# Performance work log

Hardware: AMD Instinct MI355X
Metric: run time of the kernel (lower is better)

The kernel has to match this reference:

```python
import jax, jax.numpy as jnp
import numpy as np

EPS_ATTN = 1e-6
EPS_LN = 1e-5


def _layer_norm(x, g, b):
    m = jnp.mean(x, axis=-1, keepdims=True)
    v = jnp.mean((x - m) ** 2, axis=-1, keepdims=True)
    return (x - m) * jax.lax.rsqrt(v + EPS_LN) * g + b


def _linear_attention(q, k, v):
    # q,k,v: [N, L/S, H, D]; elu feature map (+1 keeps values positive)
    q = jax.nn.elu(q) + 1.0
    k = jax.nn.elu(k) + 1.0
    s_len = v.shape[1]
    v = v / s_len
    kv = jnp.einsum('nshd,nshv->nhdv', k, v)            # [N,H,D,D]
    z = 1.0 / (jnp.einsum('nlhd,nhd->nlh', q, k.sum(axis=1)) + EPS_ATTN)
    out = jnp.einsum('nlhd,nhdv->nlhv', q, kv) * z[..., None] * s_len
    return out


def setup_inputs() -> dict:
    key = jax.random.key(0)
    ks = jax.random.split(key, 8)
    N, L, S, H, D = 4, 4096, 4096, 8, 64
    sc = 0.05
    return {
        'x': jax.random.normal(ks[0], (N, L, H, D), jnp.float32),
        'source': jax.random.normal(ks[1], (N, S, H, D), jnp.float32),
        'wq': jax.random.normal(ks[2], (D, D), jnp.float32) * sc,
        'wk': jax.random.normal(ks[3], (D, D), jnp.float32) * sc,
        'wv': jax.random.normal(ks[4], (D, D), jnp.float32) * sc,
        'wmerge': jax.random.normal(ks[5], (D, D), jnp.float32) * sc,
        'w1': jax.random.normal(ks[6], (2 * D, 2 * D), jnp.float32) * sc,
        'w2': jax.random.normal(ks[7], (D, 2 * D), jnp.float32) * sc,
        'g1': jnp.ones((D,), jnp.float32),
        'b1': jnp.zeros((D,), jnp.float32),
        'g2': jnp.ones((D,), jnp.float32),
        'b2': jnp.zeros((D,), jnp.float32),
    }


def reference(x, source, wq, wk, wv, wmerge, w1, w2, g1, b1, g2, b2):
    # projections (torch Linear: y = x @ W.T), applied on last dim D=d_model
    q = jnp.einsum('nlhd,ed->nlhe', x, wq)
    k = jnp.einsum('nshd,ed->nshe', source, wk)
    v = jnp.einsum('nshd,ed->nshe', source, wv)
    message = _linear_attention(q, k, v)                # [N,L,H,D]
    message = jnp.einsum('nlhd,ed->nlhe', message, wmerge)
    message = _layer_norm(message, g1, b1)
    h = jnp.concatenate([x, message], axis=-1)          # [N,L,H,2D]
    h = jax.nn.relu(jnp.einsum('nlhd,ed->nlhe', h, w1))
    h = jnp.einsum('nlhd,ed->nlhe', h, w2)              # [N,L,H,D]
    h = _layer_norm(h, g2, b2)
    return x + h
```

## Files before the change

### kernel.cpp

```cpp
#include <hip/hip_runtime.h>
#include <cstdint>

#define NB 4
#define LL 4096
#define SS 4096
#define HH 8
#define DD 64
#define NHC (NB*HH)
#define KVCH 16

typedef unsigned short ushort_t;
typedef __bf16 bf16x8 __attribute__((ext_vector_type(8)));
typedef float f32x4 __attribute__((ext_vector_type(4)));
typedef unsigned short u16x8 __attribute__((ext_vector_type(8)));
typedef unsigned short u16x4 __attribute__((ext_vector_type(4)));

__device__ __forceinline__ float bf2f(unsigned short u) {
    union { unsigned int i; float f; } v; v.i = ((unsigned int)u) << 16; return v.f;
}
__device__ __forceinline__ unsigned short f2bf(float f) {
    union { __bf16 b; unsigned short u; } v; v.b = (__bf16)f; return v.u;
}
__device__ __forceinline__ bool input_is_bf16(const void* g1) {
    return ((const unsigned short*)g1)[0] == 0x3F80u;
}

template<bool BF16>
__device__ __forceinline__ float ldgf(const void* p, size_t i) {
    if constexpr (BF16) return bf2f(((const unsigned short*)p)[i]);
    else                return ((const float*)p)[i];
}
template<bool BF16>
__device__ __forceinline__ u16x8 ld8(const void* p, size_t i) {
    if constexpr (BF16) {
        return *reinterpret_cast<const u16x8*>((const unsigned short*)p + i);
    } else {
        const f32x4* f4 = reinterpret_cast<const f32x4*>((const float*)p + i);
        f32x4 a = f4[0], b = f4[1];
        u16x8 o;
        #pragma unroll
        for (int j = 0; j < 4; ++j) { o[j] = f2bf(a[j]); o[4 + j] = f2bf(b[j]); }
        return o;
    }
}
__device__ __forceinline__ bf16x8 ldsA(const ushort_t* p) {
    return *reinterpret_cast<const bf16x8*>(p);
}
#define MFMA16(a,b,c) __builtin_amdgcn_mfma_f32_16x16x32_bf16(a,b,c,0,0,0)

__device__ __forceinline__ int sw64(int r, int c)  { return (r << 6) + (c ^ ((r & 7) << 3)); }
__device__ __forceinline__ int sw128(int r, int c) { return (r << 7) + (c ^ ((r & 7) << 3)); }

template<bool BF16, int LC>
__device__ __forceinline__ void stage_w(const void* g, size_t goff, ushort_t* dst,
                                        int rows, int dstride, int tid) {
    int total8 = (rows << LC) >> 3;
    for (int i8 = tid; i8 < total8; i8 += 256) {
        int i = i8 << 3;
        int r = i >> LC, c = i & ((1 << LC) - 1);
        *reinterpret_cast<u16x8*>(dst + r * dstride + c) = ld8<BF16>(g, goff + i);
    }
}
template<bool BF16, int LC, int NT>
__device__ __forceinline__ void stage_sw(const void* g, ushort_t* dst, int rows, int tid) {
    int total8 = (rows << LC) >> 3;
    for (int i8 = tid; i8 < total8; i8 += NT) {
        int i = i8 << 3;
        int r = i >> LC, c = i & ((1 << LC) - 1);
        int off;
        if constexpr (LC == 6) off = sw64(r, c); else off = sw128(r, c);
        *reinterpret_cast<u16x8*>(dst + off) = ld8<BF16>(g, i);
    }
}

__device__ __forceinline__ void red16(float v[4]) {
    #pragma unroll
    for (int m = 1; m < 16; m <<= 1) {
        #pragma unroll
        for (int r = 0; r < 4; ++r) v[r] += __shfl_xor(v[r], m);
    }
}

template<bool BF16, bool PART>
__device__ void kv_body(const void* __restrict__ src, const void* __restrict__ wk,
                        const void* __restrict__ wv, float* __restrict__ kvg,
                        float* __restrict__ ksumg,
                        ushort_t* S, ushort_t* KT, ushort_t* VT, float* KS)
{
    const int tid = threadIdx.x;
    const int lane = tid & 63, w = tid >> 6;
    const int lg = lane >> 4, l15 = lane & 15;
    const int bid = blockIdx.x;
    const int nh = bid >> 4, ch = bid & 15;
    const int n = nh >> 3, h = nh & 7;
    const int s0 = ch * 256;
    const f32x4 z4 = {0.f, 0.f, 0.f, 0.f};

    stage_w<BF16, 6>(wk, 0, KT, 64, 136, tid);
    stage_w<BF16, 6>(wv, 0, VT, 64, 136, tid);
    for (int i8 = tid; i8 < 1024; i8 += 256) {
        int r = i8 >> 3, c8 = (i8 & 7) << 3;
        size_t gb = ((size_t)((size_t)n * SS + (s0 + r)) * HH + h) * DD + c8;
        *reinterpret_cast<u16x8*>(S + r * 72 + c8) = ld8<BF16>(src, gb);
    }
    __syncthreads();

    bf16x8 wkf[2][4], wvf[2][4];
    #pragma unroll
    for (int ks = 0; ks < 2; ++ks)
        #pragma unroll
        for (int nt = 0; nt < 4; ++nt) {
            wkf[ks][nt] = ldsA(KT + (nt * 16 + l15) * 136 + ks * 32 + lg * 8);
            wvf[ks][nt] = ldsA(VT + (nt * 16 + l15) * 136 + ks * 32 + lg * 8);
        }
    __syncthreads();

    f32x4 kvacc[4];
    #pragma unroll
    for (int nt = 0; nt < 4; ++nt) kvacc[nt] = z4;
    float ksp[4] = {0.f, 0.f, 0.f, 0.f};

    for (int st = 0; st < 2; ++st) {
        #pragma unroll
        for (int mtt = 0; mtt < 2; ++mtt) {
            const int rowA = w * 32 + mtt * 16;
            bf16x8 af[2];
            #pragma unroll
            for (int ks = 0; ks < 2; ++ks)
                af[ks] = ldsA(S + (rowA + l15) * 72 + ks * 32 + lg * 8);
            f32x4 ka[4], va[4];
            #pragma unroll
            for (int nt = 0; nt < 4; ++nt) { ka[nt] = z4; va[nt] = z4; }
            __builtin_amdgcn_s_setprio(1);
            #pragma unroll
            for (int ks = 0; ks < 2; ++ks)
                #pragma unroll
                for (int nt = 0; nt < 4; ++nt) {
                    ka[nt] = MFMA16(af[ks], wkf[ks][nt], ka[nt]);
                    va[nt] = MFMA16(af[ks], wvf[ks][nt], va[nt]);
                }
            __builtin_amdgcn_s_setprio(0);
            #pragma unroll
            for (int nt = 0; nt < 4; ++nt) {
                u16x4 kp, vp;
                #pragma unroll
                for (int r = 0; r < 4; ++r) {
                    float kvl = ka[nt][r];
                    kvl = kvl > 0.f ? kvl + 1.f : __expf(kvl);
                    ksp[nt] += kvl;
                    kp[r] = f2bf(kvl);
                    vp[r] = f2bf(va[nt][r]);
                }
                const int dcol = nt * 16 + l15;
                *reinterpret_cast<u16x4*>(KT + dcol * 136 + rowA + lg * 4) = kp;
                *reinterpret_cast<u16x4*>(VT + dcol * 136 + rowA + lg * 4) = vp;
            }
        }
        __syncthreads();

        if (st == 0) {
            for (int i8 = tid; i8 < 1024; i8 += 256) {
                int r = i8 >> 3, c8 = (i8 & 7) << 3;
                size_t gb = ((size_t)((size_t)n * SS + (s0 + 128 + r)) * HH + h) * DD + c8;
                *reinterpret_cast<u16x8*>(S + r * 72 + c8) = ld8<BF16>(src, gb);
            }
        }
        __builtin_amdgcn_s_setprio(1);
        #pragma unroll
        for (int ks = 0; ks < 4; ++ks) {
            bf16x8 akv = ldsA(KT + (w * 16 + l15) * 136 + ks * 32 + lg * 8);
            #pragma unroll
            for (int nt = 0; nt < 4; ++nt) {
                bf16x8 bkv = ldsA(VT + (nt * 16 + l15) * 136 + ks * 32 + lg * 8);
                kvacc[nt] = MFMA16(akv, bkv, kvacc[nt]);
            }
        }
        __builtin_amdgcn_s_setprio(0);
        __syncthreads();
    }

    if constexpr (PART) {
        float* kvo = kvg + (size_t)bid * 4096;
        #pragma unroll
        for (int nt = 0; nt < 4; ++nt)
            #pragma unroll
            for (int r = 0; r < 4; ++r)
                kvo[(w * 16 + lg * 4 + r) * DD + nt * 16 + l15] = kvacc[nt][r];
    } else {
        float* kvo = kvg + (size_t)nh * 4096;
        #pragma unroll
        for (int nt = 0; nt < 4; ++nt)
            #pragma unroll
            for (int r = 0; r < 4; ++r)
                atomicAdd(&kvo[(w * 16 + lg * 4 + r) * DD + nt * 16 + l15], kvacc[nt][r]);
    }
    #pragma unroll
    for (int m = 16; m < 64; m <<= 1)
        #pragma unroll
        for (int nt = 0; nt < 4; ++nt) ksp[nt] += __shfl_xor(ksp[nt], m);
    if (lane < 16) {
        #pragma unroll
        for (int nt = 0; nt < 4; ++nt) KS[w * 64 + nt * 16 + lane] = ksp[nt];
    }
    __syncthreads();
    if (tid < 64) {
        float s = KS[tid] + KS[64 + tid] + KS[128 + tid] + KS[192 + tid];
        if constexpr (PART) ksumg[(size_t)bid * 64 + tid] = s;
        else                atomicAdd(&ksumg[nh * 64 + tid], s);
    }
}

template<bool PART>
__global__ __launch_bounds__(256, 2) void kv_kernel(
    const void* __restrict__ src, const void* __restrict__ wk, const void* __restrict__ wv,
    const void* __restrict__ g1, float* __restrict__ kvg, float* __restrict__ ksumg)
{
    __shared__ ushort_t S[128 * 72];
    __shared__ ushort_t KT[64 * 136];
    __shared__ ushort_t VT[64 * 136];
    __shared__ float    KS[4 * 64];
    if (input_is_bf16(g1)) kv_body<true , PART>(src, wk, wv, kvg, ksumg, S, KT, VT, KS);
    else                   kv_body<false, PART>(src, wk, wv, kvg, ksumg, S, KT, VT, KS);
}

template<bool BF16, int NCH>
__device__ void reduce_body(const float* __restrict__ kvp, const float* __restrict__ ksp,
                            const void* __restrict__ wm,
                            ushort_t* __restrict__ kvmT, float* __restrict__ ksumf,
                            ushort_t* KVS, ushort_t* WMS)
{
    const int tid = threadIdx.x;
    const int lane = tid & 63, w = tid >> 6;
    const int lg = lane >> 4, l15 = lane & 15;
    const int nh = blockIdx.x;
    const f32x4 z4 = {0.f, 0.f, 0.f, 0.f};

    stage_w<BF16, 6>(wm, 0, WMS, 64, 72, tid);
    for (int i4 = tid; i4 < 1024; i4 += 256) {
        const float* base = kvp + (size_t)nh * NCH * 4096 + i4 * 4;
        f32x4 s = z4;
        #pragma unroll
        for (int c = 0; c < NCH; ++c)
            s += *reinterpret_cast<const f32x4*>(base + c * 4096);
        int d = i4 >> 4, e4 = (i4 & 15) * 4;
        u16x4 pk;
        #pragma unroll
        for (int j = 0; j < 4; ++j) pk[j] = f2bf(s[j]);
        *reinterpret_cast<u16x4*>(KVS + d * 72 + e4) = pk;
    }
    if (tid < 64) {
        float s = 0.f;
        #pragma unroll
        for (int c = 0; c < NCH; ++c) s += ksp[((size_t)nh * NCH + c) * 64 + tid];
        ksumf[nh * 64 + tid] = s;
    }
    __syncthreads();

    bf16x8 akv[2];
    #pragma unroll
    for (int ks = 0; ks < 2; ++ks)
        akv[ks] = ldsA(KVS + (w * 16 + l15) * 72 + ks * 32 + lg * 8);
    f32x4 km[4];
    #pragma unroll
    for (int nt = 0; nt < 4; ++nt) km[nt] = z4;
    #pragma unroll
    for (int ks = 0; ks < 2; ++ks)
        #pragma unroll
        for (int nt = 0; nt < 4; ++nt) {
            bf16x8 bwm = ldsA(WMS + (nt * 16 + l15) * 72 + ks * 32 + lg * 8);
            km[nt] = MFMA16(akv[ks], bwm, km[nt]);
        }
    #pragma unroll
    for (int nt = 0; nt < 4; ++nt) {
        u16x4 pk;
        #pragma unroll
        for (int r = 0; r < 4; ++r) pk[r] = f2bf(km[nt][r]);
        *reinterpret_cast<u16x4*>(kvmT + (size_t)nh * 4096 + (nt * 16 + l15) * 64
                                  + w * 16 + lg * 4) = pk;
    }
}

template<int NCH>
__global__ __launch_bounds__(256, 4) void reduce_kernel(
    const float* __restrict__ kvp, const float* __restrict__ ksp,
    const void* __restrict__ wm, const void* __restrict__ g1,
    ushort_t* __restrict__ kvmT, float* __restrict__ ksumf)
{
    __shared__ ushort_t KVS[64 * 72];
    __shared__ ushort_t WMS[64 * 72];
    if (input_is_bf16(g1)) reduce_body<true , NCH>(kvp, ksp, wm, kvmT, ksumf, KVS, WMS);
    else                   reduce_body<false, NCH>(kvp, ksp, wm, kvmT, ksumf, KVS, WMS);
}

template<bool BF16>
__device__ void main_body(const void* __restrict__ x,
                          const void* __restrict__ wq,
                          const void* __restrict__ w1, const void* __restrict__ w2,
                          const void* __restrict__ g1, const void* __restrict__ b1,
                          const void* __restrict__ g2, const void* __restrict__ b2,
                          const ushort_t* __restrict__ kvmT,
                          const float* __restrict__ ksumf,
                          void* __restrict__ outp,
                          ushort_t* W1S, ushort_t* W2S, ushort_t* WQS,
                          ushort_t* KVMS, ushort_t* B0, ushort_t* B1, ushort_t* B2)
{
    const int tid = threadIdx.x;
    const int lane = tid & 63, w = tid >> 6;
    const int lg = lane >> 4, l15 = lane & 15;
    const int bid = blockIdx.x;
    const int nh = bid >> 3, ch = bid & 7;
    const int n = nh >> 3, h = nh & 7;
    const int rowA = w * 16;
    const f32x4 z4 = {0.f, 0.f, 0.f, 0.f};

    auto ldx = [&](int p, u16x8 xv[2]) {
        #pragma unroll
        for (int pp = 0; pp < 2; ++pp) {
            int r16 = pp * 8 + (lane >> 3), c8 = (lane & 7) << 3;
            size_t gb = ((size_t)((size_t)n * LL + (ch * 512 + p * 256 + rowA + r16)) * HH + h) * DD + c8;
            xv[pp] = ld8<BF16>(x, gb);
        }
    };

    u16x8 xv[2];
    ldx(0, xv);

    stage_sw<BF16, 6, 1024>(wq, WQS, 64, tid);
    stage_sw<BF16, 7, 1024>(w2, W2S, 64, tid);
    stage_sw<BF16, 7, 1024>(w1, W1S, 128, tid);
    stage_sw<true, 6, 1024>((const void*)(kvmT + (size_t)nh * 4096), KVMS, 64, tid);
    float g1r[4], b1r[4], g2r[4], b2r[4], ksr[4];
    #pragma unroll
    for (int nt = 0; nt < 4; ++nt) {
        int c = nt * 16 + l15;
        g1r[nt] = ldgf<BF16>(g1, c); b1r[nt] = ldgf<BF16>(b1, c);
        g2r[nt] = ldgf<BF16>(g2, c); b2r[nt] = ldgf<BF16>(b2, c);
        ksr[nt] = ksumf[nh * 64 + c];
    }
    __syncthreads();

    for (int p = 0; p < 2; ++p) {
        const int l0 = ch * 512 + p * 256;

        #pragma unroll
        for (int pp = 0; pp < 2; ++pp) {
            int r16 = pp * 8 + (lane >> 3), c8 = (lane & 7) << 3;
            *reinterpret_cast<u16x8*>(B0 + sw64(rowA + r16, c8)) = xv[pp];
        }
        u16x8 xn[2];
        if (p == 0) ldx(1, xn);

        bf16x8 af[2];
        #pragma unroll
        for (int ks = 0; ks < 2; ++ks)
            af[ks] = ldsA(B0 + sw64(rowA + l15, ks * 32 + lg * 8));
        f32x4 qa[4];
        #pragma unroll
        for (int nt = 0; nt < 4; ++nt) qa[nt] = z4;
        __builtin_amdgcn_s_setprio(1);
        #pragma unroll
        for (int ks = 0; ks < 2; ++ks)
            #pragma unroll
            for (int nt = 0; nt < 4; ++nt)
                qa[nt] = MFMA16(af[ks], ldsA(WQS + sw64(nt * 16 + l15, ks * 32 + lg * 8)), qa[nt]);
        __builtin_amdgcn_s_setprio(0);
        float zp[4] = {0.f, 0.f, 0.f, 0.f};
        #pragma unroll
        for (int nt = 0; nt < 4; ++nt)
            #pragma unroll
            for (int r = 0; r < 4; ++r) {
                float v = qa[nt][r];
                v = v > 0.f ? v + 1.f : __expf(v);
                zp[r] += v * ksr[nt];
                B1[sw64(rowA + lg * 4 + r, nt * 16 + l15)] = f2bf(v);
            }
        red16(zp);
        float zr[4];
        #pragma unroll
        for (int r = 0; r < 4; ++r) zr[r] = 1.f / (zp[r] + 1e-6f);

        #pragma unroll
        for (int ks = 0; ks < 2; ++ks)
            af[ks] = ldsA(B1 + sw64(rowA + l15, ks * 32 + lg * 8));
        f32x4 ma[4];
        #pragma unroll
        for (int nt = 0; nt < 4; ++nt) ma[nt] = z4;
        __builtin_amdgcn_s_setprio(1);
        #pragma unroll
        for (int ks = 0; ks < 2; ++ks)
            #pragma unroll
            for (int nt = 0; nt < 4; ++nt)
                ma[nt] = MFMA16(af[ks], ldsA(KVMS + sw64(nt * 16 + l15, ks * 32 + lg * 8)), ma[nt]);
        __builtin_amdgcn_s_setprio(0);
        #pragma unroll
        for (int nt = 0; nt < 4; ++nt)
            #pragma unroll
            for (int r = 0; r < 4; ++r) ma[nt][r] *= zr[r];

        float s1[4] = {0.f,0.f,0.f,0.f}, s2[4] = {0.f,0.f,0.f,0.f};
        #pragma unroll
        for (int nt = 0; nt < 4; ++nt)
            #pragma unroll
            for (int r = 0; r < 4; ++r) {
                float v = ma[nt][r]; s1[r] += v; s2[r] += v * v;
            }
        red16(s1); red16(s2);
        #pragma unroll
        for (int r = 0; r < 4; ++r) {
            float mu = s1[r] * 0.015625f;
            float var = s2[r] * 0.015625f - mu * mu;
            s1[r] = mu; s2[r] = rsqrtf(var + 1e-5f);
        }
        #pragma unroll
        for (int nt = 0; nt < 4; ++nt)
            #pragma unroll
            for (int r = 0; r < 4; ++r)
                B1[sw64(rowA + lg * 4 + r, nt * 16 + l15)] =
                    f2bf((ma[nt][r] - s1[r]) * s2[r] * g1r[nt] + b1r[nt]);

        f32x4 ha[4];
        #pragma unroll
        for (int nt = 0; nt < 4; ++nt) ha[nt] = z4;
        #pragma unroll
        for (int q = 0; q < 4; ++q) {
            f32x4 ta[2];
            ta[0] = z4; ta[1] = z4;
            __builtin_amdgcn_s_setprio(1);
            #pragma unroll
            for (int ks = 0; ks < 4; ++ks) {
                const ushort_t* bp = (ks < 2) ? B0 : B1;
                bf16x8 a1 = ldsA(bp + sw64(rowA + l15, (ks & 1) * 32 + lg * 8));
                #pragma unroll
                for (int nt = 0; nt < 2; ++nt)
                    ta[nt] = MFMA16(a1, ldsA(W1S + sw128(q * 32 + nt * 16 + l15, ks * 32 + lg * 8)), ta[nt]);
            }
            __builtin_amdgcn_s_setprio(0);
            #pragma unroll
            for (int nt = 0; nt < 2; ++nt)
                #pragma unroll
                for (int r = 0; r < 4; ++r)
                    B2[(rowA + lg * 4 + r) * 40 + nt * 16 + l15] =
                        f2bf(fmaxf(ta[nt][r], 0.f));
            bf16x8 a2 = ldsA(B2 + (rowA + l15) * 40 + lg * 8);
            __builtin_amdgcn_s_setprio(1);
            #pragma unroll
            for (int nt = 0; nt < 4; ++nt)
                ha[nt] = MFMA16(a2, ldsA(W2S + sw128(nt * 16 + l15, q * 32 + lg * 8)), ha[nt]);
            __builtin_amdgcn_s_setprio(0);
        }

        float t1[4] = {0.f,0.f,0.f,0.f}, t2[4] = {0.f,0.f,0.f,0.f};
        #pragma unroll
        for (int nt = 0; nt < 4; ++nt)
            #pragma unroll
            for (int r = 0; r < 4; ++r) {
                float v = ha[nt][r]; t1[r] += v; t2[r] += v * v;
            }
        red16(t1); red16(t2);
        #pragma unroll
        for (int r = 0; r < 4; ++r) {
            float mu = t1[r] * 0.015625f;
            float var = t2[r] * 0.015625f - mu * mu;
            t1[r] = mu; t2[r] = rsqrtf(var + 1e-5f);
        }
        #pragma unroll
        for (int nt = 0; nt < 4; ++nt)
            #pragma unroll
            for (int r = 0; r < 4; ++r) {
                float xv2 = bf2f(B0[sw64(rowA + lg * 4 + r, nt * 16 + l15)]);
                float ov = xv2 + (ha[nt][r] - t1[r]) * t2[r] * g2r[nt] + b2r[nt];
                B1[sw64(rowA + lg * 4 + r, nt * 16 + l15)] = f2bf(ov);
            }

        #pragma unroll
        for (int pp = 0; pp < 2; ++pp) {
            int r16 = pp * 8 + (lane >> 3), c8 = (lane & 7) << 3;
            size_t gb = ((size_t)((size_t)n * LL + (l0 + rowA + r16)) * HH + h) * DD + c8;
            u16x8 v = *reinterpret_cast<const u16x8*>(B1 + sw64(rowA + r16, c8));
            if constexpr (BF16) {
                *reinterpret_cast<u16x8*>((unsigned short*)outp + gb) = v;
            } else {
                float* fo = (float*)outp + gb;
                f32x4 lo, hi;
                #pragma unroll
                for (int j = 0; j < 4; ++j) { lo[j] = bf2f(v[j]); hi[j] = bf2f(v[4 + j]); }
                *reinterpret_cast<f32x4*>(fo) = lo;
                *reinterpret_cast<f32x4*>(fo + 4) = hi;
            }
        }

        if (p == 0) { xv[0] = xn[0]; xv[1] = xn[1]; }
    }
}

__global__ __launch_bounds__(1024) void main_kernel(
    const void* __restrict__ x,
    const void* __restrict__ wq,
    const void* __restrict__ w1, const void* __restrict__ w2,
    const void* __restrict__ g1, const void* __restrict__ b1,
    const void* __restrict__ g2, const void* __restrict__ b2,
    const ushort_t* __restrict__ kvmT, const float* __restrict__ ksumf,
    void* __restrict__ outp)
{
    __shared__ ushort_t W1S[128 * 128];
    __shared__ ushort_t W2S[64 * 128];
    __shared__ ushort_t WQS[64 * 64];
    __shared__ ushort_t KVMS[64 * 64];
    __shared__ ushort_t B0[256 * 64];
    __shared__ ushort_t B1[256 * 64];
    __shared__ ushort_t B2[256 * 40];
    if (input_is_bf16(g1))
        main_body<true >(x, wq, w1, w2, g1, b1, g2, b2, kvmT, ksumf, outp,
                         W1S, W2S, WQS, KVMS, B0, B1, B2);
    else
        main_body<false>(x, wq, w1, w2, g1, b1, g2, b2, kvmT, ksumf, outp,
                         W1S, W2S, WQS, KVMS, B0, B1, B2);
}

extern "C" void kernel_launch(void* const* d_in, const int* in_sizes, int n_in,
                              void* d_out, int out_size, void* d_ws, size_t ws_size,
                              hipStream_t stream) {
    const void* x   = d_in[0];
    const void* src = d_in[1];
    const void* wq  = d_in[2];
    const void* wk  = d_in[3];
    const void* wv  = d_in[4];
    const void* wm  = d_in[5];
    const void* w1  = d_in[6];
    const void* w2  = d_in[7];
    const void* g1  = d_in[8];
    const void* b1  = d_in[9];
    const void* g2  = d_in[10];
    const void* b2  = d_in[11];

    const size_t kv16   = (size_t)NHC * KVCH * 4096;
    const size_t ks16   = (size_t)NHC * KVCH * 64;
    const size_t need16 = (kv16 + ks16) * sizeof(float) + (size_t)NHC * 4096 * 2
                        + (size_t)NHC * 64 * sizeof(float);

    if (ws_size >= need16) {
        float*    kvp   = (float*)d_ws;
        float*    ksp   = kvp + kv16;
        ushort_t* kvmT  = (ushort_t*)(ksp + ks16);
        float*    ksumf = (float*)(kvmT + (size_t)NHC * 4096);
        kv_kernel<true ><<<NHC * KVCH, 256, 0, stream>>>(src, wk, wv, g1, kvp, ksp);
        reduce_kernel<KVCH><<<NHC, 256, 0, stream>>>(kvp, ksp, wm, g1, kvmT, ksumf);
        main_kernel<<<NHC * 8, 1024, 0, stream>>>(x, wq, w1, w2, g1, b1, g2, b2,
                                                  kvmT, ksumf, d_out);
    } else {
        const size_t kv1 = (size_t)NHC * 4096;
        const size_t ks1 = (size_t)NHC * 64;
        float*    kvp   = (float*)d_ws;
        float*    ksp   = kvp + kv1;
        ushort_t* kvmT  = (ushort_t*)(ksp + ks1);
        float*    ksumf = (float*)(kvmT + (size_t)NHC * 4096);
        hipMemsetAsync(d_ws, 0, (kv1 + ks1) * sizeof(float), stream);
        kv_kernel<false><<<NHC * KVCH, 256, 0, stream>>>(src, wk, wv, g1, kvp, ksp);
        reduce_kernel<1><<<NHC, 256, 0, stream>>>(kvp, ksp, wm, g1, kvmT, ksumf);
        main_kernel<<<NHC * 8, 1024, 0, stream>>>(x, wq, w1, w2, g1, b1, g2, b2,
                                                  kvmT, ksumf, d_out);
    }
}
```

Baseline: 167.5 us.

## Restructure main kernel to 512 threads with 32 rows per wave and register-held weights

The main kernel moves from 1024-thread blocks (16 rows per wave) to 512-thread blocks that each process 32 rows per wave with two M-tiles. The Wq and kv-merge B-fragments are held in registers instead of shared memory, which frees LDS and targets two blocks per CU. The reduce kernel is split into 4x more single-wave blocks that read the weights directly from global memory, removing its LDS staging and barrier. The x prefetch double-buffering is dropped, and the higher register pressure may limit occupancy.

```diff
diff --git a/kernel.cpp b/kernel.cpp
--- a/kernel.cpp
+++ b/kernel.cpp
@@ -226,40 +226,35 @@
 template<bool BF16, int NCH>
 __device__ void reduce_body(const float* __restrict__ kvp, const float* __restrict__ ksp,
                             const void* __restrict__ wm,
-                            ushort_t* __restrict__ kvmT, float* __restrict__ ksumf,
-                            ushort_t* KVS, ushort_t* WMS)
+                            ushort_t* __restrict__ kvmT, float* __restrict__ ksumf)
 {
-    const int tid = threadIdx.x;
-    const int lane = tid & 63, w = tid >> 6;
+    const int lane = threadIdx.x & 63;
     const int lg = lane >> 4, l15 = lane & 15;
-    const int nh = blockIdx.x;
+    const int bid = blockIdx.x;
+    const int nh = bid >> 2, q4 = bid & 3;
+    const int d0 = q4 * 16;
     const f32x4 z4 = {0.f, 0.f, 0.f, 0.f};
 
-    stage_w<BF16, 6>(wm, 0, WMS, 64, 72, tid);
-    for (int i4 = tid; i4 < 1024; i4 += 256) {
-        const float* base = kvp + (size_t)nh * NCH * 4096 + i4 * 4;
-        f32x4 s = z4;
-        #pragma unroll
-        for (int c = 0; c < NCH; ++c)
-            s += *reinterpret_cast<const f32x4*>(base + c * 4096);
-        int d = i4 >> 4, e4 = (i4 & 15) * 4;
-        u16x4 pk;
-        #pragma unroll
-        for (int j = 0; j < 4; ++j) pk[j] = f2bf(s[j]);
-        *reinterpret_cast<u16x4*>(KVS + d * 72 + e4) = pk;
-    }
-    if (tid < 64) {
-        float s = 0.f;
-        #pragma unroll
-        for (int c = 0; c < NCH; ++c) s += ksp[((size_t)nh * NCH + c) * 64 + tid];
-        ksumf[nh * 64 + tid] = s;
-    }
-    __syncthreads();
-
-    bf16x8 akv[2];
+    f32x4 sa[2][2];
+    #pragma unroll
+    for (int ks = 0; ks < 2; ++ks) { sa[ks][0] = z4; sa[ks][1] = z4; }
+    #pragma unroll
+    for (int c = 0; c < NCH; ++c) {
+        const float* base = kvp + ((size_t)nh * NCH + c) * 4096 + (d0 + l15) * 64;
+        #pragma unroll
+        for (int ks = 0; ks < 2; ++ks) {
+            const f32x4* p4 = reinterpret_cast<const f32x4*>(base + ks * 32 + lg * 8);
+            sa[ks][0] += p4[0];
+            sa[ks][1] += p4[1];
+        }
+    }
+    bf16x8 af[2];
     #pragma unroll
     for (int ks = 0; ks < 2; ++ks)
-        akv[ks] = ldsA(KVS + (w * 16 + l15) * 72 + ks * 32 + lg * 8);
+        #pragma unroll
+        for (int j = 0; j < 8; ++j)
+            af[ks][j] = (__bf16)((j < 4) ? sa[ks][0][j] : sa[ks][1][j - 4]);
+
     f32x4 km[4];
     #pragma unroll
     for (int nt = 0; nt < 4; ++nt) km[nt] = z4;
@@ -267,8 +262,9 @@
     for (int ks = 0; ks < 2; ++ks)
         #pragma unroll
         for (int nt = 0; nt < 4; ++nt) {
-            bf16x8 bwm = ldsA(WMS + (nt * 16 + l15) * 72 + ks * 32 + lg * 8);
-            km[nt] = MFMA16(akv[ks], bwm, km[nt]);
+            u16x8 t = ld8<BF16>(wm, (size_t)(nt * 16 + l15) * 64 + ks * 32 + lg * 8);
+            bf16x8 bwm = *reinterpret_cast<bf16x8*>(&t);
+            km[nt] = MFMA16(af[ks], bwm, km[nt]);
         }
     #pragma unroll
     for (int nt = 0; nt < 4; ++nt) {
@@ -276,20 +272,25 @@
         #pragma unroll
         for (int r = 0; r < 4; ++r) pk[r] = f2bf(km[nt][r]);
         *reinterpret_cast<u16x4*>(kvmT + (size_t)nh * 4096 + (nt * 16 + l15) * 64
-                                  + w * 16 + lg * 4) = pk;
+                                  + d0 + lg * 4) = pk;
+    }
+
+    if (q4 == 0) {
+        float s = 0.f;
+        #pragma unroll
+        for (int c = 0; c < NCH; ++c) s += ksp[((size_t)nh * NCH + c) * 64 + lane];
+        ksumf[nh * 64 + lane] = s;
     }
 }
 
 template<int NCH>
-__global__ __launch_bounds__(256, 4) void reduce_kernel(
+__global__ __launch_bounds__(64) void reduce_kernel(
     const float* __restrict__ kvp, const float* __restrict__ ksp,
     const void* __restrict__ wm, const void* __restrict__ g1,
     ushort_t* __restrict__ kvmT, float* __restrict__ ksumf)
 {
-    __shared__ ushort_t KVS[64 * 72];
-    __shared__ ushort_t WMS[64 * 72];
-    if (input_is_bf16(g1)) reduce_body<true , NCH>(kvp, ksp, wm, kvmT, ksumf, KVS, WMS);
-    else                   reduce_body<false, NCH>(kvp, ksp, wm, kvmT, ksumf, KVS, WMS);
+    if (input_is_bf16(g1)) reduce_body<true , NCH>(kvp, ksp, wm, kvmT, ksumf);
+    else                   reduce_body<false, NCH>(kvp, ksp, wm, kvmT, ksumf);
 }
 
 template<bool BF16>
@@ -301,8 +302,8 @@
                           const ushort_t* __restrict__ kvmT,
                           const float* __restrict__ ksumf,
                           void* __restrict__ outp,
-                          ushort_t* W1S, ushort_t* W2S, ushort_t* WQS,
-                          ushort_t* KVMS, ushort_t* B0, ushort_t* B1, ushort_t* B2)
+                          ushort_t* W1S, ushort_t* W2S, ushort_t* B0, ushort_t* B1,
+                          ushort_t* B2)
 {
     const int tid = threadIdx.x;
     const int lane = tid & 63, w = tid >> 6;
@@ -310,25 +311,23 @@
     const int bid = blockIdx.x;
     const int nh = bid >> 3, ch = bid & 7;
     const int n = nh >> 3, h = nh & 7;
-    const int rowA = w * 16;
+    const int rowA = w * 32;
     const f32x4 z4 = {0.f, 0.f, 0.f, 0.f};
 
-    auto ldx = [&](int p, u16x8 xv[2]) {
-        #pragma unroll
-        for (int pp = 0; pp < 2; ++pp) {
-            int r16 = pp * 8 + (lane >> 3), c8 = (lane & 7) << 3;
-            size_t gb = ((size_t)((size_t)n * LL + (ch * 512 + p * 256 + rowA + r16)) * HH + h) * DD + c8;
-            xv[pp] = ld8<BF16>(x, gb);
-        }
-    };
-
-    u16x8 xv[2];
-    ldx(0, xv);
-
-    stage_sw<BF16, 6, 1024>(wq, WQS, 64, tid);
-    stage_sw<BF16, 7, 1024>(w2, W2S, 64, tid);
-    stage_sw<BF16, 7, 1024>(w1, W1S, 128, tid);
-    stage_sw<true, 6, 1024>((const void*)(kvmT + (size_t)nh * 4096), KVMS, 64, tid);
+    stage_sw<BF16, 6, 512>(wq, B0, 64, tid);
+    stage_sw<BF16, 7, 512>(w2, W2S, 64, tid);
+    stage_sw<BF16, 7, 512>(w1, W1S, 128, tid);
+    __syncthreads();
+
+    bf16x8 wqf[2][4], kvmf[2][4];
+    #pragma unroll
+    for (int ks = 0; ks < 2; ++ks)
+        #pragma unroll
+        for (int nt = 0; nt < 4; ++nt) {
+            wqf[ks][nt] = ldsA(B0 + sw64(nt * 16 + l15, ks * 32 + lg * 8));
+            kvmf[ks][nt] = *reinterpret_cast<const bf16x8*>(
+                kvmT + (size_t)nh * 4096 + (nt * 16 + l15) * 64 + ks * 32 + lg * 8);
+        }
     float g1r[4], b1r[4], g2r[4], b2r[4], ksr[4];
     #pragma unroll
     for (int nt = 0; nt < 4; ++nt) {
@@ -342,141 +341,174 @@
     for (int p = 0; p < 2; ++p) {
         const int l0 = ch * 512 + p * 256;
 
-        #pragma unroll
-        for (int pp = 0; pp < 2; ++pp) {
-            int r16 = pp * 8 + (lane >> 3), c8 = (lane & 7) << 3;
-            *reinterpret_cast<u16x8*>(B0 + sw64(rowA + r16, c8)) = xv[pp];
-        }
-        u16x8 xn[2];
-        if (p == 0) ldx(1, xn);
-
-        bf16x8 af[2];
+        for (int i = 0; i < 4; ++i) {
+            int r = rowA + i * 8 + (lane >> 3), c8 = (lane & 7) << 3;
+            size_t gb = ((size_t)((size_t)n * LL + (l0 + r)) * HH + h) * DD + c8;
+            *reinterpret_cast<u16x8*>(B0 + sw64(r, c8)) = ld8<BF16>(x, gb);
+        }
+
+        bf16x8 af[2][2];
+        #pragma unroll
+        for (int m = 0; m < 2; ++m)
+            #pragma unroll
+            for (int ks = 0; ks < 2; ++ks)
+                af[m][ks] = ldsA(B0 + sw64(rowA + m * 16 + l15, ks * 32 + lg * 8));
+        f32x4 qa[2][4];
+        #pragma unroll
+        for (int m = 0; m < 2; ++m)
+            #pragma unroll
+            for (int nt = 0; nt < 4; ++nt) qa[m][nt] = z4;
+        __builtin_amdgcn_s_setprio(1);
         #pragma unroll
         for (int ks = 0; ks < 2; ++ks)
-            af[ks] = ldsA(B0 + sw64(rowA + l15, ks * 32 + lg * 8));
-        f32x4 qa[4];
-        #pragma unroll
-        for (int nt = 0; nt < 4; ++nt) qa[nt] = z4;
+            #pragma unroll
+            for (int nt = 0; nt < 4; ++nt) {
+                qa[0][nt] = MFMA16(af[0][ks], wqf[ks][nt], qa[0][nt]);
+                qa[1][nt] = MFMA16(af[1][ks], wqf[ks][nt], qa[1][nt]);
+            }
+        __builtin_amdgcn_s_setprio(0);
+        float zp[2][4] = {{0.f,0.f,0.f,0.f},{0.f,0.f,0.f,0.f}};
+        #pragma unroll
+        for (int m = 0; m < 2; ++m)
+            #pragma unroll
+            for (int nt = 0; nt < 4; ++nt)
+                #pragma unroll
+                for (int r = 0; r < 4; ++r) {
+                    float v = qa[m][nt][r];
+                    v = v > 0.f ? v + 1.f : __expf(v);
+                    zp[m][r] += v * ksr[nt];
+                    B1[sw64(rowA + m * 16 + lg * 4 + r, nt * 16 + l15)] = f2bf(v);
+                }
+        red16(zp[0]); red16(zp[1]);
+        float zr[2][4];
+        #pragma unroll
+        for (int m = 0; m < 2; ++m)
+            #pragma unroll
+            for (int r = 0; r < 4; ++r) zr[m][r] = 1.f / (zp[m][r] + 1e-6f);
+
+        #pragma unroll
+        for (int m = 0; m < 2; ++m)
+            #pragma unroll
+            for (int ks = 0; ks < 2; ++ks)
+                af[m][ks] = ldsA(B1 + sw64(rowA + m * 16 + l15, ks * 32 + lg * 8));
+        f32x4 ma[2][4];
+        #pragma unroll
+        for (int m = 0; m < 2; ++m)
+            #pragma unroll
+            for (int nt = 0; nt < 4; ++nt) ma[m][nt] = z4;
         __builtin_amdgcn_s_setprio(1);
         #pragma unroll
         for (int ks = 0; ks < 2; ++ks)
             #pragma unroll
+            for (int nt = 0; nt < 4; ++nt) {
+                ma[0][nt] = MFMA16(af[0][ks], kvmf[ks][nt], ma[0][nt]);
+                ma[1][nt] = MFMA16(af[1][ks], kvmf[ks][nt], ma[1][nt]);
+            }
+        __builtin_amdgcn_s_setprio(0);
+        #pragma unroll
+        for (int m = 0; m < 2; ++m)
+            #pragma unroll
             for (int nt = 0; nt < 4; ++nt)
-                qa[nt] = MFMA16(af[ks], ldsA(WQS + sw64(nt * 16 + l15, ks * 32 + lg * 8)), qa[nt]);
-        __builtin_amdgcn_s_setprio(0);
-        float zp[4] = {0.f, 0.f, 0.f, 0.f};
-        #pragma unroll
-        for (int nt = 0; nt < 4; ++nt)
+                #pragma unroll
+                for (int r = 0; r < 4; ++r) ma[m][nt][r] *= zr[m][r];
+
+        #pragma unroll
+        for (int m = 0; m < 2; ++m) {
+            float s1[4] = {0.f,0.f,0.f,0.f}, s2[4] = {0.f,0.f,0.f,0.f};
+            #pragma unroll
+            for (int nt = 0; nt < 4; ++nt)
+                #pragma unroll
+                for (int r = 0; r < 4; ++r) {
+                    float v = ma[m][nt][r]; s1[r] += v; s2[r] += v * v;
+                }
+            red16(s1); red16(s2);
             #pragma unroll
             for (int r = 0; r < 4; ++r) {
-                float v = qa[nt][r];
-                v = v > 0.f ? v + 1.f : __expf(v);
-                zp[r] += v * ksr[nt];
-                B1[sw64(rowA + lg * 4 + r, nt * 16 + l15)] = f2bf(v);
-            }
-        red16(zp);
-        float zr[4];
-        #pragma unroll
-        for (int r = 0; r < 4; ++r) zr[r] = 1.f / (zp[r] + 1e-6f);
-
-        #pragma unroll
-        for (int ks = 0; ks < 2; ++ks)
-            af[ks] = ldsA(B1 + sw64(rowA + l15, ks * 32 + lg * 8));
-        f32x4 ma[4];
-        #pragma unroll
-        for (int nt = 0; nt < 4; ++nt) ma[nt] = z4;
-        __builtin_amdgcn_s_setprio(1);
-        #pragma unroll
-        for (int ks = 0; ks < 2; ++ks)
+                float mu = s1[r] * 0.015625f;
+                float var = s2[r] * 0.015625f - mu * mu;
+                s1[r] = mu; s2[r] = rsqrtf(var + 1e-5f);
+            }
             #pragma unroll
             for (int nt = 0; nt < 4; ++nt)
-                ma[nt] = MFMA16(af[ks], ldsA(KVMS + sw64(nt * 16 + l15, ks * 32 + lg * 8)), ma[nt]);
-        __builtin_amdgcn_s_setprio(0);
-        #pragma unroll
-        for (int nt = 0; nt < 4; ++nt)
-            #pragma unroll
-            for (int r = 0; r < 4; ++r) ma[nt][r] *= zr[r];
-
-        float s1[4] = {0.f,0.f,0.f,0.f}, s2[4] = {0.f,0.f,0.f,0.f};
-        #pragma unroll
-        for (int nt = 0; nt < 4; ++nt)
-            #pragma unroll
-            for (int r = 0; r < 4; ++r) {
-                float v = ma[nt][r]; s1[r] += v; s2[r] += v * v;
-            }
-        red16(s1); red16(s2);
-        #pragma unroll
-        for (int r = 0; r < 4; ++r) {
-            float mu = s1[r] * 0.015625f;
-            float var = s2[r] * 0.015625f - mu * mu;
-            s1[r] = mu; s2[r] = rsqrtf(var + 1e-5f);
-        }
-        #pragma unroll
-        for (int nt = 0; nt < 4; ++nt)
-            #pragma unroll
-            for (int r = 0; r < 4; ++r)
-                B1[sw64(rowA + lg * 4 + r, nt * 16 + l15)] =
-                    f2bf((ma[nt][r] - s1[r]) * s2[r] * g1r[nt] + b1r[nt]);
-
-        f32x4 ha[4];
-        #pragma unroll
-        for (int nt = 0; nt < 4; ++nt) ha[nt] = z4;
+                #pragma unroll
+                for (int r = 0; r < 4; ++r)
+                    B1[sw64(rowA + m * 16 + lg * 4 + r, nt * 16 + l15)] =
+                        f2bf((ma[m][nt][r] - s1[r]) * s2[r] * g1r[nt] + b1r[nt]);
+        }
+
+        f32x4 ha[2][4];
+        #pragma unroll
+        for (int m = 0; m < 2; ++m)
+            #pragma unroll
+            for (int nt = 0; nt < 4; ++nt) ha[m][nt] = z4;
         #pragma unroll
         for (int q = 0; q < 4; ++q) {
-            f32x4 ta[2];
-            ta[0] = z4; ta[1] = z4;
+            f32x4 ta[2][2];
+            #pragma unroll
+            for (int m = 0; m < 2; ++m) { ta[m][0] = z4; ta[m][1] = z4; }
             __builtin_amdgcn_s_setprio(1);
             #pragma unroll
             for (int ks = 0; ks < 4; ++ks) {
                 const ushort_t* bp = (ks < 2) ? B0 : B1;
-                bf16x8 a1 = ldsA(bp + sw64(rowA + l15, (ks & 1) * 32 + lg * 8));
+                bf16x8 a10 = ldsA(bp + sw64(rowA + l15, (ks & 1) * 32 + lg * 8));
+                bf16x8 a11 = ldsA(bp + sw64(rowA + 16 + l15, (ks & 1) * 32 + lg * 8));
+                #pragma unroll
+                for (int nt = 0; nt < 2; ++nt) {
+                    bf16x8 bw = ldsA(W1S + sw128(q * 32 + nt * 16 + l15, ks * 32 + lg * 8));
+                    ta[0][nt] = MFMA16(a10, bw, ta[0][nt]);
+                    ta[1][nt] = MFMA16(a11, bw, ta[1][nt]);
+                }
+            }
+            __builtin_amdgcn_s_setprio(0);
+            #pragma unroll
+            for (int m = 0; m < 2; ++m)
                 #pragma unroll
                 for (int nt = 0; nt < 2; ++nt)
-                    ta[nt] = MFMA16(a1, ldsA(W1S + sw128(q * 32 + nt * 16 + l15, ks * 32 + lg * 8)), ta[nt]);
+                    #pragma unroll
+                    for (int r = 0; r < 4; ++r)
+                        B2[(rowA + m * 16 + lg * 4 + r) * 40 + nt * 16 + l15] =
+                            f2bf(fmaxf(ta[m][nt][r], 0.f));
+            bf16x8 a20 = ldsA(B2 + (rowA + l15) * 40 + lg * 8);
+            bf16x8 a21 = ldsA(B2 + (rowA + 16 + l15) * 40 + lg * 8);
+            __builtin_amdgcn_s_setprio(1);
+            #pragma unroll
+            for (int nt = 0; nt < 4; ++nt) {
+                bf16x8 w2b = ldsA(W2S + sw128(nt * 16 + l15, q * 32 + lg * 8));
+                ha[0][nt] = MFMA16(a20, w2b, ha[0][nt]);
+                ha[1][nt] = MFMA16(a21, w2b, ha[1][nt]);
             }
             __builtin_amdgcn_s_setprio(0);
-            #pragma unroll
-            for (int nt = 0; nt < 2; ++nt)
-                #pragma unroll
-                for (int r = 0; r < 4; ++r)
-                    B2[(rowA + lg * 4 + r) * 40 + nt * 16 + l15] =
-                        f2bf(fmaxf(ta[nt][r], 0.f));
-            bf16x8 a2 = ldsA(B2 + (rowA + l15) * 40 + lg * 8);
-            __builtin_amdgcn_s_setprio(1);
+        }
+
+        #pragma unroll
+        for (int m = 0; m < 2; ++m) {
+            float t1[4] = {0.f,0.f,0.f,0.f}, t2[4] = {0.f,0.f,0.f,0.f};
             #pragma unroll
             for (int nt = 0; nt < 4; ++nt)
-                ha[nt] = MFMA16(a2, ldsA(W2S + sw128(nt * 16 + l15, q * 32 + lg * 8)), ha[nt]);
-            __builtin_amdgcn_s_setprio(0);
-        }
-
-        float t1[4] = {0.f,0.f,0.f,0.f}, t2[4] = {0.f,0.f,0.f,0.f};
-        #pragma unroll
-        for (int nt = 0; nt < 4; ++nt)
+                #pragma unroll
+                for (int r = 0; r < 4; ++r) {
+                    float v = ha[m][nt][r]; t1[r] += v; t2[r] += v * v;
+                }
+            red16(t1); red16(t2);
             #pragma unroll
             for (int r = 0; r < 4; ++r) {
-                float v = ha[nt][r]; t1[r] += v; t2[r] += v * v;
-            }
-        red16(t1); red16(t2);
-        #pragma unroll
-        for (int r = 0; r < 4; ++r) {
-            float mu = t1[r] * 0.015625f;
-            float var = t2[r] * 0.015625f - mu * mu;
-            t1[r] = mu; t2[r] = rsqrtf(var + 1e-5f);
-        }
-        #pragma unroll
-        for (int nt = 0; nt < 4; ++nt)
-            #pragma unroll
-            for (int r = 0; r < 4; ++r) {
-                float xv2 = bf2f(B0[sw64(rowA + lg * 4 + r, nt * 16 + l15)]);
-                float ov = xv2 + (ha[nt][r] - t1[r]) * t2[r] * g2r[nt] + b2r[nt];
-                B1[sw64(rowA + lg * 4 + r, nt * 16 + l15)] = f2bf(ov);
-            }
-
-        #pragma unroll
-        for (int pp = 0; pp < 2; ++pp) {
-            int r16 = pp * 8 + (lane >> 3), c8 = (lane & 7) << 3;
-            size_t gb = ((size_t)((size_t)n * LL + (l0 + rowA + r16)) * HH + h) * DD + c8;
-            u16x8 v = *reinterpret_cast<const u16x8*>(B1 + sw64(rowA + r16, c8));
+                float mu = t1[r] * 0.015625f;
+                float var = t2[r] * 0.015625f - mu * mu;
+                t1[r] = mu; t2[r] = rsqrtf(var + 1e-5f);
+            }
+            #pragma unroll
+            for (int nt = 0; nt < 4; ++nt)
+                #pragma unroll
+                for (int r = 0; r < 4; ++r) {
+                    float xv2 = bf2f(B0[sw64(rowA + m * 16 + lg * 4 + r, nt * 16 + l15)]);
+                    float ov = xv2 + (ha[m][nt][r] - t1[r]) * t2[r] * g2r[nt] + b2r[nt];
+                    B1[sw64(rowA + m * 16 + lg * 4 + r, nt * 16 + l15)] = f2bf(ov);
+                }
+        }
+        for (int i = 0; i < 4; ++i) {
+            int r = rowA + i * 8 + (lane >> 3), c8 = (lane & 7) << 3;
+            size_t gb = ((size_t)((size_t)n * LL + (l0 + r)) * HH + h) * DD + c8;
+            u16x8 v = *reinterpret_cast<const u16x8*>(B1 + sw64(r, c8));
             if constexpr (BF16) {
                 *reinterpret_cast<u16x8*>((unsigned short*)outp + gb) = v;
             } else {
@@ -488,12 +520,10 @@
                 *reinterpret_cast<f32x4*>(fo + 4) = hi;
             }
         }
-
-        if (p == 0) { xv[0] = xn[0]; xv[1] = xn[1]; }
-    }
-}
-
-__global__ __launch_bounds__(1024) void main_kernel(
+    }
+}
+
+__global__ __launch_bounds__(512, 2) void main_kernel(
     const void* __restrict__ x,
     const void* __restrict__ wq,
     const void* __restrict__ w1, const void* __restrict__ w2,
@@ -504,17 +534,15 @@
 {
     __shared__ ushort_t W1S[128 * 128];
     __shared__ ushort_t W2S[64 * 128];
-    __shared__ ushort_t WQS[64 * 64];
-    __shared__ ushort_t KVMS[64 * 64];
     __shared__ ushort_t B0[256 * 64];
     __shared__ ushort_t B1[256 * 64];
     __shared__ ushort_t B2[256 * 40];
     if (input_is_bf16(g1))
         main_body<true >(x, wq, w1, w2, g1, b1, g2, b2, kvmT, ksumf, outp,
-                         W1S, W2S, WQS, KVMS, B0, B1, B2);
+                         W1S, W2S, B0, B1, B2);
     else
         main_body<false>(x, wq, w1, w2, g1, b1, g2, b2, kvmT, ksumf, outp,
-                         W1S, W2S, WQS, KVMS, B0, B1, B2);
+                         W1S, W2S, B0, B1, B2);
 }
 
 extern "C" void kernel_launch(void* const* d_in, const int* in_sizes, int n_in,
@@ -544,9 +572,9 @@
         ushort_t* kvmT  = (ushort_t*)(ksp + ks16);
         float*    ksumf = (float*)(kvmT + (size_t)NHC * 4096);
         kv_kernel<true ><<<NHC * KVCH, 256, 0, stream>>>(src, wk, wv, g1, kvp, ksp);
-        reduce_kernel<KVCH><<<NHC, 256, 0, stream>>>(kvp, ksp, wm, g1, kvmT, ksumf);
-        main_kernel<<<NHC * 8, 1024, 0, stream>>>(x, wq, w1, w2, g1, b1, g2, b2,
-                                                  kvmT, ksumf, d_out);
+        reduce_kernel<KVCH><<<NHC * 4, 64, 0, stream>>>(kvp, ksp, wm, g1, kvmT, ksumf);
+        main_kernel<<<NHC * 8, 512, 0, stream>>>(x, wq, w1, w2, g1, b1, g2, b2,
+                                                 kvmT, ksumf, d_out);
     } else {
         const size_t kv1 = (size_t)NHC * 4096;
         const size_t ks1 = (size_t)NHC * 64;
@@ -556,8 +584,8 @@
         float*    ksumf = (float*)(kvmT + (size_t)NHC * 4096);
         hipMemsetAsync(d_ws, 0, (kv1 + ks1) * sizeof(float), stream);
         kv_kernel<false><<<NHC * KVCH, 256, 0, stream>>>(src, wk, wv, g1, kvp, ksp);
-        reduce_kernel<1><<<NHC, 256, 0, stream>>>(kvp, ksp, wm, g1, kvmT, ksumf);
-        main_kernel<<<NHC * 8, 1024, 0, stream>>>(x, wq, w1, w2, g1, b1, g2, b2,
-                                                  kvmT, ksumf, d_out);
-    }
-}
+        reduce_kernel<1><<<NHC * 4, 64, 0, stream>>>(kvp, ksp, wm, g1, kvmT, ksumf);
+        main_kernel<<<NHC * 8, 512, 0, stream>>>(x, wq, w1, w2, g1, b1, g2, b2,
+                                                 kvmT, ksumf, d_out);
+    }
+}
```

Result: slower. 172.2 us (+2.9%).
